# Performance work log

Hardware: AMD Instinct MI355X
Metric: run time of the kernel (lower is better)

The kernel has to match this reference:

```python
import jax, jax.numpy as jnp
import numpy as np

DELTA_V = 0.5
DELTA_D = 1.5
ALPHA = 1.0
BETA = 1.0
GAMMA = 0.001
K = 33  # label ids 0..32; 0 = background (ignored)
EPS = 1e-12


def setup_inputs() -> dict:
    key = jax.random.key(0)
    k1, k2 = jax.random.split(key)
    B, N, E = 8, 65536, 32
    embeddings = jax.random.normal(k1, (B, N, E), dtype=jnp.float32)
    labels = jax.random.randint(k2, (B, N), 0, K)
    return {"embeddings": embeddings, "labels": labels}


def reference(embeddings, labels):
    B, N, E = embeddings.shape
    dt = embeddings.dtype
    seg = (labels + jnp.arange(B)[:, None] * K).reshape(-1)  # (B*N,)

    # segment mean -> per-instance centers (B, K, E)
    sums = jax.ops.segment_sum(embeddings.reshape(B * N, E), seg, num_segments=B * K).reshape(B, K, E)
    counts = jax.ops.segment_sum(jnp.ones((B * N,), dtype=dt), seg, num_segments=B * K).reshape(B, K)
    centers = sums / jnp.maximum(counts, 1.0)[..., None]

    present = counts > 0
    present = present.at[:, 0].set(False)  # drop background label 0
    presf = present.astype(dt)
    n_inst = presf.sum(axis=1)  # (B,)

    # ---- variance term: per-point hinge distance to own center, segment-mean ----
    c_per_point = centers[jnp.arange(B)[:, None], labels]  # (B, N, E) gather
    d2 = ((embeddings - c_per_point) ** 2).sum(-1)
    dist = jnp.sqrt(jnp.maximum(d2, EPS))
    hinge = jnp.where(labels > 0, jnp.maximum(dist - DELTA_V, 0.0), 0.0)
    per_inst_sum = jax.ops.segment_sum(hinge.reshape(-1), seg, num_segments=B * K).reshape(B, K)
    per_inst_mean = per_inst_sum / jnp.maximum(counts, 1.0)
    variance_term = (per_inst_mean * presf).sum(1) / jnp.maximum(n_inst, 1.0)

    # ---- distance term: pairwise hinge between present instance centers ----
    diff2 = ((centers[:, :, None, :] - centers[:, None, :, :]) ** 2).sum(-1)  # (B,K,K)
    upper = jnp.triu(jnp.ones((K, K), dtype=bool), 1)[None]
    pair_valid = present[:, :, None] & present[:, None, :] & upper
    cd = jnp.sqrt(jnp.maximum(jnp.where(pair_valid, diff2, 1.0), EPS))
    pair_hinge = jnp.maximum(2.0 * DELTA_D - cd, 0.0) * pair_valid.astype(dt)
    n_pairs = n_inst * (n_inst - 1.0) * 0.5
    distance_term = pair_hinge.sum((1, 2)) / jnp.maximum(n_pairs, 1.0)

    # ---- regularization: mean L2 norm of present centers ----
    c_norm = jnp.sqrt(jnp.maximum((centers ** 2).sum(-1), EPS))
    reg_term = (c_norm * presf).sum(1) / jnp.maximum(n_inst, 1.0)

    per_batch = ALPHA * variance_term + BETA * distance_term + GAMMA * reg_term
    per_batch = jnp.where(n_inst > 0, per_batch, 0.0)
    return per_batch.sum() / B
```

## Files before the change

### kernel.cpp

```cpp
#include <hip/hip_runtime.h>
#include <math.h>

#define KC 33
#define ED 32
#define KE (KC * ED)
#define PAD 33

#define BPB_A 128
#define BPB_H 128


__global__ void k_zero(float* __restrict__ ws, int n, float* __restrict__ out) {
    int i = blockIdx.x * blockDim.x + threadIdx.x;
    if (i < n) ws[i] = 0.f;
    if (i == 0) out[0] = 0.f;
}

__global__ __launch_bounds__(256) void k_accum(const float* __restrict__ emb,
                                               const int* __restrict__ lab,
                                               float* __restrict__ sums,
                                               float* __restrict__ counts, int N) {
    __shared__ float s_stage[8 * 4 * PAD];
    __shared__ float s_priv[8 * KE];
    __shared__ unsigned short s_lab[512];
    __shared__ float s_hist[2 * KC];
    int t = threadIdx.x;
    int b     = blockIdx.x / BPB_A;
    int blk   = blockIdx.x % BPB_A;
    int chunk = N / BPB_A;
    int e  = t & 31;
    int s  = t >> 5;
    int w  = t >> 6;
    int h  = (t >> 5) & 1;
    int l5 = t & 31;
    size_t pbase = (size_t)b * N + (size_t)blk * chunk;
    const float4* g4 = (const float4*)(emb + pbase * ED);

    for (int i = t; i < 8 * KE; i += 256) s_priv[i] = 0.f;
    if (t < 2 * KC) s_hist[t] = 0.f;

    int2 lp = ((const int2*)(lab + pbase))[t];
    s_lab[2 * t]     = (unsigned short)lp.x;
    s_lab[2 * t + 1] = (unsigned short)lp.y;
    __syncthreads();
    {
        float* hh = &s_hist[(t >> 7) * KC];
        atomicAdd(&hh[lp.x], 1.f);
        atomicAdd(&hh[lp.y], 1.f);
    }

    float* strip = &s_stage[s * 4 * PAD];
    float* priv  = &s_priv[s * KE];
    int fbase = w * 1024 + h * 32 + l5;
    float4 cur = g4[fbase];
    for (int g = 0; g < 16; g++) {
        {
            float* d = &strip[(l5 >> 3) * PAD + (l5 & 7) * 4];
            d[0] = cur.x; d[1] = cur.y; d[2] = cur.z; d[3] = cur.w;
        }
        if (g + 1 < 16) cur = g4[fbase + (g + 1) * 64];
        int lbase = w * 128 + g * 8 + h * 4;
#pragma unroll
        for (int j = 0; j < 4; j++) {
            float x = strip[j * PAD + e];
            int   k = (int)s_lab[lbase + j];
            priv[k * ED + e] += x;
        }
    }
    __syncthreads();

    for (int i = t; i < KE; i += 256) {
        float v = 0.f;
#pragma unroll
        for (int c = 0; c < 8; c++) v += s_priv[c * KE + i];
        atomicAdd(&sums[(size_t)b * KE + i], v);
    }
    if (t < KC)
        atomicAdd(&counts[b * KC + t], s_hist[t] + s_hist[KC + t]);
}

__global__ __launch_bounds__(256) void k_hinge(const float* __restrict__ emb,
                                               const int* __restrict__ lab,
                                               const float* __restrict__ sums,
                                               const float* __restrict__ counts,
                                               float* __restrict__ var, int N) {
    __shared__ float s_wtile[4 * 64 * PAD];
    __shared__ float s_ctr[KC * PAD];
    __shared__ float s_cnt[KC];
    __shared__ float s_inv[KC];
    __shared__ unsigned short s_lab[512];
    __shared__ float s_red[4];
    int t = threadIdx.x;
    int b     = blockIdx.x / BPB_H;
    int blk   = blockIdx.x % BPB_H;
    int chunk = N / BPB_H;
    int w = t >> 6, l = t & 63;
    size_t pbase = (size_t)b * N + (size_t)blk * chunk;
    const float4* g4 = (const float4*)(emb + pbase * ED);

    int2 lp = ((const int2*)(lab + pbase))[t];
    s_lab[2 * t]     = (unsigned short)lp.x;
    s_lab[2 * t + 1] = (unsigned short)lp.y;

    if (t < KC) {
        float c = counts[b * KC + t];
        s_cnt[t] = fmaxf(c, 1.f);
        s_inv[t] = (t > 0 && c > 0.f) ? 1.f / fmaxf(c, 1.f) : 0.f;
    }
    __syncthreads();
    for (int i = t; i < KE; i += 256) {
        int k = i >> 5, e = i & 31;
        s_ctr[k * PAD + e] = sums[(size_t)b * KE + i] / s_cnt[k];
    }
    __syncthreads();

    float* strip = &s_wtile[w * 64 * PAD];
    int fb = w * 1024 + l;
    float4 r0 = g4[fb],       r1 = g4[fb + 64],  r2 = g4[fb + 128], r3 = g4[fb + 192];
    float4 r4 = g4[fb + 256], r5 = g4[fb + 320], r6 = g4[fb + 384], r7 = g4[fb + 448];

    float hs = 0.f;
    for (int g = 0; g < 2; g++) {
        {
            int f, p, m;
            f = l;        p = f >> 3; m = (f & 7) * 4;
            { float* d = &strip[PAD * p + m]; d[0]=r0.x; d[1]=r0.y; d[2]=r0.z; d[3]=r0.w; }
            f = l + 64;   p = f >> 3; m = (f & 7) * 4;
            { float* d = &strip[PAD * p + m]; d[0]=r1.x; d[1]=r1.y; d[2]=r1.z; d[3]=r1.w; }
            f = l + 128;  p = f >> 3; m = (f & 7) * 4;
            { float* d = &strip[PAD * p + m]; d[0]=r2.x; d[1]=r2.y; d[2]=r2.z; d[3]=r2.w; }
            f = l + 192;  p = f >> 3; m = (f & 7) * 4;
            { float* d = &strip[PAD * p + m]; d[0]=r3.x; d[1]=r3.y; d[2]=r3.z; d[3]=r3.w; }
            f = l + 256;  p = f >> 3; m = (f & 7) * 4;
            { float* d = &strip[PAD * p + m]; d[0]=r4.x; d[1]=r4.y; d[2]=r4.z; d[3]=r4.w; }
            f = l + 320;  p = f >> 3; m = (f & 7) * 4;
            { float* d = &strip[PAD * p + m]; d[0]=r5.x; d[1]=r5.y; d[2]=r5.z; d[3]=r5.w; }
            f = l + 384;  p = f >> 3; m = (f & 7) * 4;
            { float* d = &strip[PAD * p + m]; d[0]=r6.x; d[1]=r6.y; d[2]=r6.z; d[3]=r6.w; }
            f = l + 448;  p = f >> 3; m = (f & 7) * 4;
            { float* d = &strip[PAD * p + m]; d[0]=r7.x; d[1]=r7.y; d[2]=r7.z; d[3]=r7.w; }
        }
        if (g + 1 < 2) {
            int nb = fb + 512;
            r0 = g4[nb];       r1 = g4[nb + 64];  r2 = g4[nb + 128]; r3 = g4[nb + 192];
            r4 = g4[nb + 256]; r5 = g4[nb + 320]; r6 = g4[nb + 384]; r7 = g4[nb + 448];
        }

        int   k  = (int)s_lab[w * 128 + g * 64 + l];
        float iv = s_inv[k];
        const float* xr = &strip[l * PAD];
        const float* cr = &s_ctr[k * PAD];
        float d2 = 0.f;
#pragma unroll
        for (int j = 0; j < ED; j++) {
            float d = xr[j] - cr[j];
            d2 = fmaf(d, d, d2);
        }
        float dist = sqrtf(fmaxf(d2, 1e-12f));
        hs += fmaxf(dist - 0.5f, 0.f) * iv;
    }

    hs += __shfl_xor(hs, 1);  hs += __shfl_xor(hs, 2);  hs += __shfl_xor(hs, 4);
    hs += __shfl_xor(hs, 8);  hs += __shfl_xor(hs, 16); hs += __shfl_xor(hs, 32);
    if ((t & 63) == 0) s_red[t >> 6] = hs;
    __syncthreads();
    if (t == 0)
        atomicAdd(&var[b], s_red[0] + s_red[1] + s_red[2] + s_red[3]);
}

__global__ __launch_bounds__(256) void k_final(const float* __restrict__ sums,
                                               const float* __restrict__ counts,
                                               const float* __restrict__ var,
                                               float* __restrict__ out, int B) {
    __shared__ float s_ctr[KE];
    __shared__ float s_cnt[KC];
    __shared__ float s_reg[KC];
    __shared__ int   s_prs[KC];
    __shared__ float s_red[256];
    int b = blockIdx.x;
    int t = threadIdx.x;

    if (t < KC) {
        float c = counts[b * KC + t];
        s_cnt[t] = fmaxf(c, 1.f);
        s_prs[t] = (t > 0 && c > 0.f) ? 1 : 0;
    }
    __syncthreads();
    for (int i = t; i < KE; i += 256)
        s_ctr[i] = sums[(size_t)b * KE + i] / s_cnt[i >> 5];
    __syncthreads();
    if (t < KC) {
        float n2 = 0.f;
        for (int e2 = 0; e2 < ED; e2++) { float c = s_ctr[t * ED + e2]; n2 += c * c; }
        s_reg[t] = s_prs[t] ? sqrtf(fmaxf(n2, 1e-12f)) : 0.f;
    }
    __syncthreads();

    float psum = 0.f;
    for (int q = t; q < KC * KC; q += 256) {
        int i = q / KC, j = q % KC;
        if (i < j && s_prs[i] && s_prs[j]) {
            float d2 = 0.f;
            for (int e2 = 0; e2 < ED; e2++) {
                float d = s_ctr[i * ED + e2] - s_ctr[j * ED + e2];
                d2 += d * d;
            }
            float cd = sqrtf(fmaxf(d2, 1e-12f));
            psum += fmaxf(3.0f - cd, 0.f);
        }
    }
    s_red[t] = psum;
    __syncthreads();
    for (int s = 128; s > 0; s >>= 1) {
        if (t < s) s_red[t] += s_red[t + s];
        __syncthreads();
    }

    if (t == 0) {
        float reg = 0.f; int n = 0;
        for (int k = 0; k < KC; k++) { reg += s_reg[k]; n += s_prs[k]; }
        float nf = (float)n;
        float variance_term = var[b] / fmaxf(nf, 1.f);
        float npairs = nf * (nf - 1.f) * 0.5f;
        float distance_term = s_red[0] / fmaxf(npairs, 1.f);
        float reg_term = reg / fmaxf(nf, 1.f);
        float pb = variance_term + distance_term + 0.001f * reg_term;
        if (n == 0) pb = 0.f;
        atomicAdd(out, pb / (float)B);
    }
}

extern "C" void kernel_launch(void* const* d_in, const int* in_sizes, int n_in,
                              void* d_out, int out_size, void* d_ws, size_t ws_size,
                              hipStream_t stream) {
    const float* emb = (const float*)d_in[0];
    const int*   lab = (const int*)d_in[1];
    float* out = (float*)d_out;

    const int B = 8;
    const int N = in_sizes[1] / B;

    float* sums   = (float*)d_ws;
    float* counts = sums + (size_t)B * KE;
    float* var    = counts + (size_t)B * KC;

    int zn = B * KE + B * KC + B;
    k_zero<<<(zn + 255) / 256, 256, 0, stream>>>(sums, zn, out);
    k_accum<<<B * BPB_A, 256, 0, stream>>>(emb, lab, sums, counts, N);
    k_hinge<<<B * BPB_H, 256, 0, stream>>>(emb, lab, sums, counts, var, N);
    k_final<<<B, 256, 0, stream>>>(sums, counts, var, out, B);
}
```

Before: 127.8 us.

## Replace global atomics with per-block partials and a deterministic center-reduction kernel

Each k_accum block now writes its partial sums and counts to its own slot in workspace instead of using atomicAdd. A new k_centers kernel reduces those partials, computes the centers once, and stores them along with the counts. The zero-init kernel goes away, and the hinge and final kernels read precomputed centers and per-block variance partials, with k_final now a single block looping over the batches. The accum loop also prefetches two float4 loads ahead instead of one. This removes contended atomics and the zeroing launch, at the cost of an extra kernel and more workspace traffic.

```diff
diff --git a/kernel.cpp b/kernel.cpp
--- a/kernel.cpp
+++ b/kernel.cpp
@@ -8,25 +8,21 @@
 
 #define BPB_A 128
 #define BPB_H 128
-
-
-__global__ void k_zero(float* __restrict__ ws, int n, float* __restrict__ out) {
-    int i = blockIdx.x * blockDim.x + threadIdx.x;
-    if (i < n) ws[i] = 0.f;
-    if (i == 0) out[0] = 0.f;
-}
+#define QD 264
+
 
 __global__ __launch_bounds__(256) void k_accum(const float* __restrict__ emb,
                                                const int* __restrict__ lab,
-                                               float* __restrict__ sums,
-                                               float* __restrict__ counts, int N) {
+                                               float* __restrict__ psums,
+                                               float* __restrict__ pcnt, int N) {
     __shared__ float s_stage[8 * 4 * PAD];
     __shared__ float s_priv[8 * KE];
     __shared__ unsigned short s_lab[512];
     __shared__ float s_hist[2 * KC];
     int t = threadIdx.x;
-    int b     = blockIdx.x / BPB_A;
-    int blk   = blockIdx.x % BPB_A;
+    int bid   = blockIdx.x;
+    int b     = bid / BPB_A;
+    int blk   = bid % BPB_A;
     int chunk = N / BPB_A;
     int e  = t & 31;
     int s  = t >> 5;
@@ -52,13 +48,15 @@
     float* strip = &s_stage[s * 4 * PAD];
     float* priv  = &s_priv[s * KE];
     int fbase = w * 1024 + h * 32 + l5;
-    float4 cur = g4[fbase];
+    float4 c0 = g4[fbase];
+    float4 c1 = g4[fbase + 64];
     for (int g = 0; g < 16; g++) {
         {
             float* d = &strip[(l5 >> 3) * PAD + (l5 & 7) * 4];
-            d[0] = cur.x; d[1] = cur.y; d[2] = cur.z; d[3] = cur.w;
-        }
-        if (g + 1 < 16) cur = g4[fbase + (g + 1) * 64];
+            d[0] = c0.x; d[1] = c0.y; d[2] = c0.z; d[3] = c0.w;
+        }
+        float4 c2;
+        if (g + 2 < 16) c2 = g4[fbase + (g + 2) * 64];
         int lbase = w * 128 + g * 8 + h * 4;
 #pragma unroll
         for (int j = 0; j < 4; j++) {
@@ -66,6 +64,7 @@
             int   k = (int)s_lab[lbase + j];
             priv[k * ED + e] += x;
         }
+        c0 = c1; c1 = c2;
     }
     __syncthreads();
 
@@ -73,20 +72,47 @@
         float v = 0.f;
 #pragma unroll
         for (int c = 0; c < 8; c++) v += s_priv[c * KE + i];
-        atomicAdd(&sums[(size_t)b * KE + i], v);
+        psums[(size_t)bid * KE + i] = v;
     }
     if (t < KC)
-        atomicAdd(&counts[b * KC + t], s_hist[t] + s_hist[KC + t]);
+        pcnt[((size_t)b * KC + t) * BPB_A + blk] = s_hist[t] + s_hist[KC + t];
+}
+
+__global__ __launch_bounds__(256) void k_centers(const float* __restrict__ psums,
+                                                 const float* __restrict__ pcnt,
+                                                 float* __restrict__ centers,
+                                                 float* __restrict__ counts) {
+    __shared__ float s_cnt[KC];
+    int t = threadIdx.x;
+    int b = blockIdx.x >> 2;
+    int q = blockIdx.x & 3;
+    if (t < KC) {
+        const float4* p4 = (const float4*)(pcnt + ((size_t)b * KC + t) * BPB_A);
+        float c = 0.f;
+        for (int u = 0; u < BPB_A / 4; u++) {
+            float4 v = p4[u];
+            c += (v.x + v.y) + (v.z + v.w);
+        }
+        s_cnt[t] = c;
+        if (q == 0) counts[b * KC + t] = c;
+    }
+    __syncthreads();
+    for (int il = t; il < QD; il += 256) {
+        int i = q * QD + il;
+        const float* ps = psums + (size_t)b * BPB_A * KE + i;
+        float acc = 0.f;
+        for (int blk = 0; blk < BPB_A; blk++) acc += ps[(size_t)blk * KE];
+        centers[(size_t)b * KE + i] = acc / fmaxf(s_cnt[i >> 5], 1.f);
+    }
 }
 
 __global__ __launch_bounds__(256) void k_hinge(const float* __restrict__ emb,
                                                const int* __restrict__ lab,
-                                               const float* __restrict__ sums,
+                                               const float* __restrict__ centers,
                                                const float* __restrict__ counts,
-                                               float* __restrict__ var, int N) {
+                                               float* __restrict__ pvar, int N) {
     __shared__ float s_wtile[4 * 64 * PAD];
     __shared__ float s_ctr[KC * PAD];
-    __shared__ float s_cnt[KC];
     __shared__ float s_inv[KC];
     __shared__ unsigned short s_lab[512];
     __shared__ float s_red[4];
@@ -104,13 +130,11 @@
 
     if (t < KC) {
         float c = counts[b * KC + t];
-        s_cnt[t] = fmaxf(c, 1.f);
         s_inv[t] = (t > 0 && c > 0.f) ? 1.f / fmaxf(c, 1.f) : 0.f;
     }
-    __syncthreads();
     for (int i = t; i < KE; i += 256) {
         int k = i >> 5, e = i & 31;
-        s_ctr[k * PAD + e] = sums[(size_t)b * KE + i] / s_cnt[k];
+        s_ctr[k * PAD + e] = centers[(size_t)b * KE + i];
     }
     __syncthreads();
 
@@ -165,69 +189,77 @@
     if ((t & 63) == 0) s_red[t >> 6] = hs;
     __syncthreads();
     if (t == 0)
-        atomicAdd(&var[b], s_red[0] + s_red[1] + s_red[2] + s_red[3]);
-}
-
-__global__ __launch_bounds__(256) void k_final(const float* __restrict__ sums,
+        pvar[blockIdx.x] = s_red[0] + s_red[1] + s_red[2] + s_red[3];
+}
+
+__global__ __launch_bounds__(256) void k_final(const float* __restrict__ centers,
                                                const float* __restrict__ counts,
-                                               const float* __restrict__ var,
+                                               const float* __restrict__ pvar,
                                                float* __restrict__ out, int B) {
     __shared__ float s_ctr[KE];
-    __shared__ float s_cnt[KC];
     __shared__ float s_reg[KC];
     __shared__ int   s_prs[KC];
     __shared__ float s_red[256];
-    int b = blockIdx.x;
-    int t = threadIdx.x;
-
-    if (t < KC) {
-        float c = counts[b * KC + t];
-        s_cnt[t] = fmaxf(c, 1.f);
-        s_prs[t] = (t > 0 && c > 0.f) ? 1 : 0;
-    }
-    __syncthreads();
-    for (int i = t; i < KE; i += 256)
-        s_ctr[i] = sums[(size_t)b * KE + i] / s_cnt[i >> 5];
-    __syncthreads();
-    if (t < KC) {
-        float n2 = 0.f;
-        for (int e2 = 0; e2 < ED; e2++) { float c = s_ctr[t * ED + e2]; n2 += c * c; }
-        s_reg[t] = s_prs[t] ? sqrtf(fmaxf(n2, 1e-12f)) : 0.f;
-    }
-    __syncthreads();
-
-    float psum = 0.f;
-    for (int q = t; q < KC * KC; q += 256) {
-        int i = q / KC, j = q % KC;
-        if (i < j && s_prs[i] && s_prs[j]) {
-            float d2 = 0.f;
-            for (int e2 = 0; e2 < ED; e2++) {
-                float d = s_ctr[i * ED + e2] - s_ctr[j * ED + e2];
-                d2 += d * d;
+    int t = threadIdx.x;
+    float total = 0.f;
+
+    for (int b = 0; b < B; b++) {
+        __syncthreads();
+        if (t < KC) {
+            float c = counts[b * KC + t];
+            s_prs[t] = (t > 0 && c > 0.f) ? 1 : 0;
+        }
+        for (int i = t; i < KE; i += 256)
+            s_ctr[i] = centers[(size_t)b * KE + i];
+        __syncthreads();
+        if (t < KC) {
+            float n2 = 0.f;
+            for (int e2 = 0; e2 < ED; e2++) { float c = s_ctr[t * ED + e2]; n2 += c * c; }
+            s_reg[t] = s_prs[t] ? sqrtf(fmaxf(n2, 1e-12f)) : 0.f;
+        }
+        s_red[t] = (t < BPB_H) ? pvar[b * BPB_H + t] : 0.f;
+        __syncthreads();
+        for (int s = 128; s > 0; s >>= 1) {
+            if (t < s) s_red[t] += s_red[t + s];
+            __syncthreads();
+        }
+        float var_b = s_red[0];
+        __syncthreads();
+
+        float psum = 0.f;
+        for (int q = t; q < KC * KC; q += 256) {
+            int i = q / KC, j = q % KC;
+            if (i < j && s_prs[i] && s_prs[j]) {
+                float d2 = 0.f;
+                for (int e2 = 0; e2 < ED; e2++) {
+                    float d = s_ctr[i * ED + e2] - s_ctr[j * ED + e2];
+                    d2 += d * d;
+                }
+                float cd = sqrtf(fmaxf(d2, 1e-12f));
+                psum += fmaxf(3.0f - cd, 0.f);
             }
-            float cd = sqrtf(fmaxf(d2, 1e-12f));
-            psum += fmaxf(3.0f - cd, 0.f);
-        }
-    }
-    s_red[t] = psum;
-    __syncthreads();
-    for (int s = 128; s > 0; s >>= 1) {
-        if (t < s) s_red[t] += s_red[t + s];
-        __syncthreads();
-    }
-
-    if (t == 0) {
-        float reg = 0.f; int n = 0;
-        for (int k = 0; k < KC; k++) { reg += s_reg[k]; n += s_prs[k]; }
-        float nf = (float)n;
-        float variance_term = var[b] / fmaxf(nf, 1.f);
-        float npairs = nf * (nf - 1.f) * 0.5f;
-        float distance_term = s_red[0] / fmaxf(npairs, 1.f);
-        float reg_term = reg / fmaxf(nf, 1.f);
-        float pb = variance_term + distance_term + 0.001f * reg_term;
-        if (n == 0) pb = 0.f;
-        atomicAdd(out, pb / (float)B);
-    }
+        }
+        s_red[t] = psum;
+        __syncthreads();
+        for (int s = 128; s > 0; s >>= 1) {
+            if (t < s) s_red[t] += s_red[t + s];
+            __syncthreads();
+        }
+
+        if (t == 0) {
+            float reg = 0.f; int n = 0;
+            for (int k = 0; k < KC; k++) { reg += s_reg[k]; n += s_prs[k]; }
+            float nf = (float)n;
+            float variance_term = var_b / fmaxf(nf, 1.f);
+            float npairs = nf * (nf - 1.f) * 0.5f;
+            float distance_term = s_red[0] / fmaxf(npairs, 1.f);
+            float reg_term = reg / fmaxf(nf, 1.f);
+            float pb = variance_term + distance_term + 0.001f * reg_term;
+            if (n == 0) pb = 0.f;
+            total += pb;
+        }
+    }
+    if (t == 0) out[0] = total / (float)B;
 }
 
 extern "C" void kernel_launch(void* const* d_in, const int* in_sizes, int n_in,
@@ -240,13 +272,14 @@
     const int B = 8;
     const int N = in_sizes[1] / B;
 
-    float* sums   = (float*)d_ws;
-    float* counts = sums + (size_t)B * KE;
-    float* var    = counts + (size_t)B * KC;
-
-    int zn = B * KE + B * KC + B;
-    k_zero<<<(zn + 255) / 256, 256, 0, stream>>>(sums, zn, out);
-    k_accum<<<B * BPB_A, 256, 0, stream>>>(emb, lab, sums, counts, N);
-    k_hinge<<<B * BPB_H, 256, 0, stream>>>(emb, lab, sums, counts, var, N);
-    k_final<<<B, 256, 0, stream>>>(sums, counts, var, out, B);
-}
+    float* psums   = (float*)d_ws;
+    float* pcnt    = psums + (size_t)B * BPB_A * KE;
+    float* pvar    = pcnt + (size_t)B * KC * BPB_A;
+    float* centers = pvar + (size_t)B * BPB_H;
+    float* counts  = centers + (size_t)B * KE;
+
+    k_accum<<<B * BPB_A, 256, 0, stream>>>(emb, lab, psums, pcnt, N);
+    k_centers<<<B * 4, 256, 0, stream>>>(psums, pcnt, centers, counts);
+    k_hinge<<<B * BPB_H, 256, 0, stream>>>(emb, lab, centers, counts, pvar, N);
+    k_final<<<1, 256, 0, stream>>>(centers, counts, pvar, out, B);
+}
```

Result: slower. 168.7 us (+32.0%).
